# Kernel tuning notes

Measured on AMD Instinct MI355X. Metric: run time of the kernel, lower is better.

The kernel has to match this reference:

```python
import math
import jax, jax.numpy as jnp
import numpy as np

B, IMG, P, D, DEPTH, NH, HD = 8, 384, 16, 768, 12, 12, 64
NREG, NS, NF = 4, 5, 16            # registers, special tokens (1 cls + 4 reg), rope freqs
HP = IMG // P                      # 24 patches per side
NPATCH = HP * HP                   # 576
ROPE_DIM = 2 * NF                  # 32
SCALE = HD ** -0.5


def setup_inputs() -> dict:
    key = jax.random.key(0)
    ks = jax.random.split(key, 12)
    s = 0.02
    rn = lambda k, shape: (jax.random.normal(k, shape, jnp.float32) * s)
    L, DF = DEPTH, 4 * D
    inp = {
        "pixel_values": jax.random.normal(ks[0], (B, 3, IMG, IMG), jnp.float32),
        "conv_w": rn(ks[1], (D, 3, P, P)),
        "conv_b": jnp.zeros((D,), jnp.float32),
        "cls_token": rn(ks[2], (1, 1, D)),
        "storage_tokens": rn(ks[3], (1, NREG, D)),
        "periods": jnp.exp(jnp.linspace(0.0, math.log(100.0), NF)).astype(jnp.float32),
        "ln1_s": jnp.ones((L, D), jnp.float32),
        "ln1_b": jnp.zeros((L, D), jnp.float32),
        "qkv_w": rn(ks[4], (L, 3 * D, D)),
        "qkv_b": rn(ks[5], (L, 3 * D)),
        "bias_mask": jnp.zeros((L, 3 * D), jnp.float32),  # buffer init zeros -> bias nulled
        "proj_w": rn(ks[6], (L, D, D)),
        "proj_b": jnp.zeros((L, D), jnp.float32),
        "ls1": jnp.ones((L, D), jnp.float32),
        "ln2_s": jnp.ones((L, D), jnp.float32),
        "ln2_b": jnp.zeros((L, D), jnp.float32),
        "fc1_w": rn(ks[7], (L, DF, D)),
        "fc1_b": jnp.zeros((L, DF), jnp.float32),
        "fc2_w": rn(ks[8], (L, D, DF)),
        "fc2_b": jnp.zeros((L, D), jnp.float32),
        "ls2": jnp.ones((L, D), jnp.float32),
        "lnf_s": jnp.ones((D,), jnp.float32),
        "lnf_b": jnp.zeros((D,), jnp.float32),
    }
    return inp


def _ln(x, s, b):
    mu = x.mean(-1, keepdims=True)
    var = ((x - mu) ** 2).mean(-1, keepdims=True)
    return (x - mu) / jnp.sqrt(var + 1e-6) * s + b


def _rot(x, cos, sin):
    # x: [b, h, n_patch, 2*NF]; cos/sin: [n_patch, NF]; interleaved even/odd rotation
    even, odd = x[..., 0::2], x[..., 1::2]
    return jnp.stack([even * cos - odd * sin, even * sin + odd * cos], axis=-1).reshape(x.shape)


def _forward(pixel_values, conv_w, conv_b, cls_token, storage_tokens, periods,
             ln1_s, ln1_b, qkv_w, qkv_b, bias_mask, proj_w, proj_b, ls1,
             ln2_s, ln2_b, fc1_w, fc1_b, fc2_w, fc2_b, ls2, lnf_s, lnf_b):
    b = pixel_values.shape[0]
    # Patch embed: stride == kernel conv as reshape + einsum
    xp = pixel_values.reshape(b, 3, HP, P, HP, P)
    tok = jnp.einsum('bchpwq,dcpq->bhwd', xp, conv_w) + conv_b       # [b,HP,HP,D]
    tok = tok.reshape(b, NPATCH, D)
    x = jnp.concatenate([jnp.broadcast_to(cls_token, (b, 1, D)),
                         jnp.broadcast_to(storage_tokens, (b, NREG, D)), tok], axis=1)
    n = x.shape[1]

    # RoPE tables (periods buffer; freqs = 2*pi / periods)
    freqs = (2.0 * math.pi) / periods                                 # [NF]
    pos = jnp.arange(HP, dtype=jnp.float32)
    gy, gx = jnp.meshgrid(pos, pos, indexing='ij')
    ax = gx.reshape(-1, 1) * freqs                                    # [NPATCH, NF]
    ay = gy.reshape(-1, 1) * freqs
    cos_x, sin_x = jnp.cos(ax), jnp.sin(ax)
    cos_y, sin_y = jnp.cos(ay), jnp.sin(ay)

    def blk(h, p):
        (l1s, l1b, qw, qb, bm, pw, pb, g1, l2s, l2b, f1w, f1b, f2w, f2b, g2) = p
        h1 = _ln(h, l1s, l1b)
        qkv = h1 @ qw.T + qb * bm                                     # bias nulled by mask
        qkv = qkv.reshape(b, n, 3, NH, HD).transpose(2, 0, 3, 1, 4)   # [3,b,NH,n,HD]
        q, k, v = qkv[0], qkv[1], qkv[2]
        # rotary on patch tokens; rope_total == HD so the whole head is rotated
        qp, kp = q[:, :, NS:], k[:, :, NS:]
        qp = jnp.concatenate([_rot(qp[..., :ROPE_DIM], cos_x, sin_x),
                              _rot(qp[..., ROPE_DIM:], cos_y, sin_y)], axis=-1)
        kp = jnp.concatenate([_rot(kp[..., :ROPE_DIM], cos_x, sin_x),
                              _rot(kp[..., ROPE_DIM:], cos_y, sin_y)], axis=-1)
        q = jnp.concatenate([q[:, :, :NS], qp], axis=2)
        k = jnp.concatenate([k[:, :, :NS], kp], axis=2)
        attn = jax.nn.softmax(jnp.einsum('bhqd,bhkd->bhqk', q, k) * SCALE, axis=-1)
        o = jnp.einsum('bhqk,bhkd->bhqd', attn, v).transpose(0, 2, 1, 3).reshape(b, n, D)
        h = h + g1 * (o @ pw.T + pb)
        h2 = _ln(h, l2s, l2b)
        m = jax.nn.gelu(h2 @ f1w.T + f1b, approximate=False) @ f2w.T + f2b
        h = h + g2 * m
        return h, None

    params = (ln1_s, ln1_b, qkv_w, qkv_b, bias_mask, proj_w, proj_b, ls1,
              ln2_s, ln2_b, fc1_w, fc1_b, fc2_w, fc2_b, ls2)
    x, _ = jax.lax.scan(blk, x, params)
    return _ln(x, lnf_s, lnf_b)


def reference(pixel_values, conv_w, conv_b, cls_token, storage_tokens, periods,
              ln1_s, ln1_b, qkv_w, qkv_b, bias_mask, proj_w, proj_b, ls1,
              ln2_s, ln2_b, fc1_w, fc1_b, fc2_w, fc2_b, ls2, lnf_s, lnf_b):
    return _forward(pixel_values, conv_w, conv_b, cls_token, storage_tokens, periods,
                    ln1_s, ln1_b, qkv_w, qkv_b, bias_mask, proj_w, proj_b, ls1,
                    ln2_s, ln2_b, fc1_w, fc1_b, fc2_w, fc2_b, ls2, lnf_s, lnf_b)
```

## Files before the change

kernel.cpp:

```cpp
#include <hip/hip_runtime.h>
#include <math.h>

typedef unsigned short u16;
typedef __attribute__((ext_vector_type(8))) short bf8;
typedef __attribute__((ext_vector_type(4))) float f4;

#define DEV static __device__ __forceinline__

DEV u16 f2b(float f){
  unsigned u = __builtin_bit_cast(unsigned, f);
  u += 0x7fffu + ((u >> 16) & 1u);
  return (u16)(u >> 16);
}
DEV float b2f(u16 h){
  unsigned u = ((unsigned)h) << 16;
  return __builtin_bit_cast(float, u);
}

#define BATCH  8
#define NTOK   581
#define NPAD   640
#define DIM    768
#define DFF    3072
#define NHEAD  12
#define HDIM   64
#define NLAYER 12
#define MTOK   (BATCH*NTOK)
#define MPAD2  4736
#define MCONV  (BATCH*576)
#define ATTN_SCALE 0.125f
#define BHEADS (BATCH*NHEAD)
#define QSZ    ((long long)BHEADS*NPAD*HDIM)

enum { EPI_CONV=0, EPI_QKV, EPI_PROJ, EPI_GELU, EPI_FC2 };

DEV int xcdswz(int lin, int n){
  int q = n >> 3, r = n & 7;
  int x = lin & 7, o = lin >> 3;
  return (x < r ? x*(q+1) : r*(q+1) + (x - r)*q) + o;
}

template<int EPI, int BM>
__global__ __launch_bounds__(256) void gemmRS(
    const u16* __restrict__ A, int lda,
    const u16* __restrict__ B, int ldb, int K,
    const float* __restrict__ bias,
    const float* __restrict__ aux,
    float* __restrict__ Cf,
    u16* __restrict__ Cb)
{
  constexpr int MR = BM / 32;
  const int gx = gridDim.x;
  const int lin = blockIdx.y * gx + blockIdx.x;
  const int tix = xcdswz(lin, gx * gridDim.y);
  const int bm = (tix / gx) * BM, bn = (tix % gx) * 64;
  __shared__ __attribute__((aligned(16))) u16 As[2][BM][40];
  __shared__ __attribute__((aligned(16))) u16 Bs[2][64][40];
  const int tid  = threadIdx.x;
  const int lane = tid & 63, wid = tid >> 6;
  const int wr = wid >> 1, wc = wid & 1;
  const int srow = tid >> 2, scol = (tid & 3) * 8;
  const u16* gA0 = A + (long long)(bm + srow) * lda + scol;
  const u16* gA1 = A + (long long)(bm + 64 + srow) * lda + scol;
  const u16* gB  = B + (long long)(bn + srow) * ldb + scol;
  const int frow = lane & 15, quad = lane >> 4, fk = quad * 8;

  f4 acc[MR][2] = {};
  const int T = K >> 5;

  auto compute = [&](int buf){
    bf8 af[MR], bf[2];
    #pragma unroll
    for (int m = 0; m < MR; ++m)
      af[m] = *(const bf8*)&As[buf][wr*(BM/2) + m*16 + frow][fk];
    #pragma unroll
    for (int n = 0; n < 2; ++n)
      bf[n] = *(const bf8*)&Bs[buf][wc*32 + n*16 + frow][fk];
    #pragma unroll
    for (int m = 0; m < MR; ++m)
    #pragma unroll
    for (int n = 0; n < 2; ++n)
      acc[m][n] = __builtin_amdgcn_mfma_f32_16x16x32_bf16(af[m], bf[n], acc[m][n], 0, 0, 0);
  };

  bf8 xA0, xA1, xB, yA0, yA1, yB;
  xA0 = *(const bf8*)gA0;        if constexpr (BM == 128) xA1 = *(const bf8*)gA1;
  xB  = *(const bf8*)gB;
  yA0 = *(const bf8*)(gA0 + 32); if constexpr (BM == 128) yA1 = *(const bf8*)(gA1 + 32);
  yB  = *(const bf8*)(gB + 32);
  *(bf8*)&As[0][srow][scol] = xA0;
  if constexpr (BM == 128) *(bf8*)&As[0][64 + srow][scol] = xA1;
  *(bf8*)&Bs[0][srow][scol] = xB;
  __syncthreads();

  for (int t = 0; t < T; t += 2){
    if (t + 2 < T){
      xA0 = *(const bf8*)(gA0 + (t+2)*32);
      if constexpr (BM == 128) xA1 = *(const bf8*)(gA1 + (t+2)*32);
      xB  = *(const bf8*)(gB  + (t+2)*32);
    }
    *(bf8*)&As[1][srow][scol] = yA0;
    if constexpr (BM == 128) *(bf8*)&As[1][64 + srow][scol] = yA1;
    *(bf8*)&Bs[1][srow][scol] = yB;
    compute(0);
    __syncthreads();
    if (t + 3 < T){
      yA0 = *(const bf8*)(gA0 + (t+3)*32);
      if constexpr (BM == 128) yA1 = *(const bf8*)(gA1 + (t+3)*32);
      yB  = *(const bf8*)(gB  + (t+3)*32);
    }
    if (t + 2 < T){
      *(bf8*)&As[0][srow][scol] = xA0;
      if constexpr (BM == 128) *(bf8*)&As[0][64 + srow][scol] = xA1;
      *(bf8*)&Bs[0][srow][scol] = xB;
    }
    compute(1);
    __syncthreads();
  }

  #pragma unroll
  for (int mi = 0; mi < MR; ++mi)
  #pragma unroll
  for (int ni = 0; ni < 2; ++ni){
    f4 v = acc[mi][ni];
    int col = bn + wc*32 + ni*16 + frow;
    int r0  = bm + wr*(BM/2) + mi*16 + quad*4;
    #pragma unroll
    for (int j = 0; j < 4; ++j){
      int m = r0 + j;
      float val = v[j];
      if constexpr (EPI == EPI_CONV){
        int b = m / 576, p = m % 576;
        Cf[((long long)b*NTOK + 5 + p)*DIM + col] = val + bias[col];
      } else if constexpr (EPI == EPI_QKV){
        if (m < MTOK){
          int b = m / NTOK, t = m % NTOK;
          int which = col / DIM, rem = col % DIM;
          int h = rem / HDIM, hd = rem % HDIM;
          float x = val + bias[col];
          long long bh = (long long)(b*NHEAD + h);
          if (which == 0) x *= ATTN_SCALE;
          if (which == 2)
            Cb[2*QSZ + (bh*HDIM + hd)*NPAD + t] = f2b(x);
          else
            Cb[(long long)which*QSZ + (bh*NPAD + t)*HDIM + hd] = f2b(x);
        }
      } else if constexpr (EPI == EPI_PROJ || EPI == EPI_FC2){
        if (m < MTOK)
          Cf[(long long)m*DIM + col] += aux[col] * (val + bias[col]);
      } else if constexpr (EPI == EPI_GELU){
        float x = val + bias[col];
        float g = 0.5f * x * (1.0f + erff(x * 0.70710678118f));
        Cb[(long long)m*DFF + col] = f2b(g);
      }
    }
  }
}

__global__ __launch_bounds__(256) void flash_k(
    const u16* __restrict__ Q, const u16* __restrict__ K,
    const u16* __restrict__ VT, u16* __restrict__ obuf)
{
  const int qb = blockIdx.x, bh = blockIdx.y;
  const int b = bh / NHEAD, h = bh % NHEAD;
  const int tid = threadIdx.x, lane = tid & 63, w = tid >> 6;
  const int frow = lane & 15, quad = lane >> 4;
  __shared__ u16 P[4][16][80];
  const u16* Qb = Q  + (long long)bh * NPAD * HDIM;
  const u16* Kb = K  + (long long)bh * NPAD * HDIM;
  const u16* Vb = VT + (long long)bh * HDIM * NPAD;
  const bf8 qa0 = *(const bf8*)&Qb[(qb*64 + w*16 + frow)*HDIM + quad*8];
  const bf8 qa1 = *(const bf8*)&Qb[(qb*64 + w*16 + frow)*HDIM + 32 + quad*8];
  f4 o[4] = {};
  float m[4], l[4];
  #pragma unroll
  for (int j = 0; j < 4; ++j){ m[j] = -1e30f; l[j] = 0.0f; }

  for (int kt = 0; kt < NPAD/64; ++kt){
    f4 s[4];
    #pragma unroll
    for (int n = 0; n < 4; ++n){
      const u16* kr = &Kb[(kt*64 + n*16 + frow)*HDIM + quad*8];
      bf8 kb0 = *(const bf8*)kr;
      bf8 kb1 = *(const bf8*)(kr + 32);
      f4 z = {};
      z    = __builtin_amdgcn_mfma_f32_16x16x32_bf16(qa0, kb0, z, 0, 0, 0);
      s[n] = __builtin_amdgcn_mfma_f32_16x16x32_bf16(qa1, kb1, z, 0, 0, 0);
    }
    if (kt == NPAD/64 - 1){
      #pragma unroll
      for (int n = 0; n < 4; ++n){
        int kcol = kt*64 + n*16 + frow;
        if (kcol >= NTOK){ s[n][0] = s[n][1] = s[n][2] = s[n][3] = -1e30f; }
      }
    }
    float sc[4];
    #pragma unroll
    for (int j = 0; j < 4; ++j){
      float v = fmaxf(fmaxf(s[0][j], s[1][j]), fmaxf(s[2][j], s[3][j]));
      v = fmaxf(v, __shfl_xor(v, 1));  v = fmaxf(v, __shfl_xor(v, 2));
      v = fmaxf(v, __shfl_xor(v, 4));  v = fmaxf(v, __shfl_xor(v, 8));
      float mn = fmaxf(m[j], v);
      sc[j] = __expf(m[j] - mn);
      m[j] = mn;
    }
    float ts[4] = {0.f, 0.f, 0.f, 0.f};
    #pragma unroll
    for (int n = 0; n < 4; ++n){
      #pragma unroll
      for (int j = 0; j < 4; ++j){
        float p = __expf(s[n][j] - m[j]);
        ts[j] += p;
        P[w][quad*4 + j][n*16 + frow] = f2b(p);
      }
    }
    #pragma unroll
    for (int j = 0; j < 4; ++j){
      float v = ts[j];
      v += __shfl_xor(v, 1); v += __shfl_xor(v, 2);
      v += __shfl_xor(v, 4); v += __shfl_xor(v, 8);
      l[j] = l[j]*sc[j] + v;
    }
    #pragma unroll
    for (int n = 0; n < 4; ++n)
    #pragma unroll
    for (int j = 0; j < 4; ++j) o[n][j] *= sc[j];
    bf8 pa0 = *(const bf8*)&P[w][frow][quad*8];
    bf8 pa1 = *(const bf8*)&P[w][frow][quad*8 + 32];
    #pragma unroll
    for (int n = 0; n < 4; ++n){
      const u16* vr = &Vb[(n*16 + frow)*NPAD + kt*64 + quad*8];
      bf8 vb0 = *(const bf8*)vr;
      bf8 vb1 = *(const bf8*)(vr + 32);
      o[n] = __builtin_amdgcn_mfma_f32_16x16x32_bf16(pa0, vb0, o[n], 0, 0, 0);
      o[n] = __builtin_amdgcn_mfma_f32_16x16x32_bf16(pa1, vb1, o[n], 0, 0, 0);
    }
  }
  #pragma unroll
  for (int j = 0; j < 4; ++j){
    int t = qb*64 + w*16 + quad*4 + j;
    if (t < NTOK){
      float inv = 1.0f / l[j];
      #pragma unroll
      for (int n = 0; n < 4; ++n)
        obuf[((long long)b*NTOK + t)*DIM + h*HDIM + n*16 + frow] = f2b(o[n][j] * inv);
    }
  }
}

template<int F32OUT>
__global__ __launch_bounds__(256) void ln_k(const float* __restrict__ x,
    const float* __restrict__ s, const float* __restrict__ b,
    u16* __restrict__ ob, float* __restrict__ of)
{
  const long long row = blockIdx.x;
  const float* xr = x + row * DIM;
  const int t = threadIdx.x;
  float v0 = xr[t], v1 = xr[t + 256], v2 = xr[t + 512];
  float sum = v0 + v1 + v2;
  #pragma unroll
  for (int o = 32; o; o >>= 1) sum += __shfl_down(sum, o);
  __shared__ float r1[4], r2[4];
  const int lane = t & 63, w = t >> 6;
  if (lane == 0) r1[w] = sum;
  __syncthreads();
  float mu = (r1[0] + r1[1] + r1[2] + r1[3]) * (1.0f / DIM);
  float d0 = v0 - mu, d1 = v1 - mu, d2 = v2 - mu;
  float vs = d0*d0 + d1*d1 + d2*d2;
  #pragma unroll
  for (int o = 32; o; o >>= 1) vs += __shfl_down(vs, o);
  if (lane == 0) r2[w] = vs;
  __syncthreads();
  float inv = 1.0f / sqrtf((r2[0] + r2[1] + r2[2] + r2[3]) * (1.0f / DIM) + 1e-6f);
  if constexpr (F32OUT){
    float* orow = of + row * DIM;
    orow[t]       = d0 * inv * s[t]       + b[t];
    orow[t + 256] = d1 * inv * s[t + 256] + b[t + 256];
    orow[t + 512] = d2 * inv * s[t + 512] + b[t + 512];
  } else {
    u16* orow = ob + row * DIM;
    orow[t]       = f2b(d0 * inv * s[t]       + b[t]);
    orow[t + 256] = f2b(d1 * inv * s[t + 256] + b[t + 256]);
    orow[t + 512] = f2b(d2 * inv * s[t + 512] + b[t + 512]);
  }
}

__global__ void ropetab_k(const float* __restrict__ periods, float* __restrict__ tab)
{
  int idx = blockIdx.x * blockDim.x + threadIdx.x;
  if (idx >= 24 * 16) return;
  int c = idx >> 4, f = idx & 15;
  float fr = 6.283185307179586f / periods[f];
  float a = (float)c * fr;
  tab[idx]       = cosf(a);
  tab[384 + idx] = sinf(a);
}

__global__ __launch_bounds__(256) void rope_k(u16* __restrict__ Q, u16* __restrict__ K,
                                              const float* __restrict__ tab)
{
  int idx = blockIdx.x * blockDim.x + threadIdx.x;
  if (idx >= BHEADS * 576 * 32) return;
  int f  = idx & 31;
  int p  = (idx >> 5) % 576;
  int bh = idx / (576 * 32);
  int px = p % 24, py = p / 24;
  float c, s; int d0;
  if (f < 16){ c = tab[px*16 + f];        s = tab[384 + px*16 + f];        d0 = 2*f; }
  else       { int ff = f - 16;
               c = tab[py*16 + ff];       s = tab[384 + py*16 + ff];       d0 = 32 + 2*ff; }
  long long off = (((long long)bh) * NPAD + 5 + p) * HDIM + d0;
  float qe = b2f(Q[off]), qo = b2f(Q[off + 1]);
  Q[off]     = f2b(qe * c - qo * s);
  Q[off + 1] = f2b(qe * s + qo * c);
  float ke = b2f(K[off]), ko = b2f(K[off + 1]);
  K[off]     = f2b(ke * c - ko * s);
  K[off + 1] = f2b(ke * s + ko * c);
}

__global__ void initx_k(float* __restrict__ x, const float* __restrict__ cls,
                        const float* __restrict__ stor)
{
  int idx = blockIdx.x * blockDim.x + threadIdx.x;
  if (idx >= BATCH * 5 * DIM) return;
  int d = idx % DIM; int t = (idx / DIM) % 5; int b = idx / (5 * DIM);
  x[((long long)b * NTOK + t) * DIM + d] = (t == 0) ? cls[d] : stor[(t - 1) * DIM + d];
}

__global__ void patch_k(const float* __restrict__ px, u16* __restrict__ Ap)
{
  int idx = blockIdx.x * blockDim.x + threadIdx.x;
  if (idx >= MCONV * DIM) return;
  int k = idx % DIM, m = idx / DIM;
  int b = m / 576, r = m % 576, hp = r / 24, wp = r % 24;
  int c = k / 256, rem = k % 256, p = rem / 16, q = rem % 16;
  float v = px[((((long long)b * 3 + c) * 384) + hp * 16 + p) * 384 + wp * 16 + q];
  Ap[idx] = f2b(v);
}

__global__ void cvt_k(const float* __restrict__ src, u16* __restrict__ dst, long long n)
{
  long long i = (long long)blockIdx.x * blockDim.x + threadIdx.x;
  long long stride = (long long)gridDim.x * blockDim.x;
  for (; i < n; i += stride) dst[i] = f2b(src[i]);
}

__global__ void biaseff_k(const float* __restrict__ qb, const float* __restrict__ bm,
                          float* __restrict__ out, int n)
{
  int i = blockIdx.x * blockDim.x + threadIdx.x;
  if (i < n) out[i] = qb[i] * bm[i];
}

extern "C" void kernel_launch(void* const* d_in, const int* in_sizes, int n_in,
                              void* d_out, int out_size, void* d_ws, size_t ws_size,
                              hipStream_t stream)
{
  const float* pixel   = (const float*)d_in[0];
  const float* conv_w  = (const float*)d_in[1];
  const float* conv_b  = (const float*)d_in[2];
  const float* cls     = (const float*)d_in[3];
  const float* stor    = (const float*)d_in[4];
  const float* periods = (const float*)d_in[5];
  const float* ln1s    = (const float*)d_in[6];
  const float* ln1b    = (const float*)d_in[7];
  const float* qkvw    = (const float*)d_in[8];
  const float* qkvb    = (const float*)d_in[9];
  const float* bmask   = (const float*)d_in[10];
  const float* projw   = (const float*)d_in[11];
  const float* projb   = (const float*)d_in[12];
  const float* ls1     = (const float*)d_in[13];
  const float* ln2s    = (const float*)d_in[14];
  const float* ln2b    = (const float*)d_in[15];
  const float* fc1w    = (const float*)d_in[16];
  const float* fc1b    = (const float*)d_in[17];
  const float* fc2w    = (const float*)d_in[18];
  const float* fc2b    = (const float*)d_in[19];
  const float* ls2     = (const float*)d_in[20];
  const float* lnfs    = (const float*)d_in[21];
  const float* lnfb    = (const float*)d_in[22];

  char* wsp = (char*)d_ws;
  auto alloc = [&](long long bytes) -> char* {
    char* p = wsp; wsp += (bytes + 255) & ~255LL; return p;
  };
  u16*   wqkv  = (u16*)  alloc((long long)NLAYER*2304*768*2);
  u16*   wproj = (u16*)  alloc((long long)NLAYER*768*768*2);
  u16*   wfc1  = (u16*)  alloc((long long)NLAYER*3072*768*2);
  u16*   wfc2  = (u16*)  alloc((long long)NLAYER*768*3072*2);
  u16*   wconv = (u16*)  alloc((long long)768*768*2);
  float* beff  = (float*)alloc((long long)NLAYER*2304*4);
  float* x     = (float*)alloc((long long)MPAD2*DIM*4);
  u16*   h     = (u16*)  alloc((long long)MPAD2*DIM*2);
  u16*   obuf  = (u16*)  alloc((long long)MPAD2*DIM*2);
  u16*   mlp   = (u16*)  alloc((long long)MPAD2*DFF*2);
  u16*   Ap    = (u16*)  alloc((long long)MCONV*DIM*2);
  u16*   Q     = (u16*)  alloc(QSZ*2*3);
  u16*   Kb    = Q + QSZ;
  u16*   VT    = Q + 2*QSZ;
  float* tab   = (float*)alloc((long long)2*24*16*4);
  if ((size_t)(wsp - (char*)d_ws) > ws_size) return;

  auto cvt = [&](const float* src, u16* dst, long long n){
    long long nb = (n + 255) / 256; if (nb > 4096) nb = 4096;
    cvt_k<<<(int)nb, 256, 0, stream>>>(src, dst, n);
  };
  cvt(qkvw,  wqkv,  (long long)NLAYER*2304*768);
  cvt(projw, wproj, (long long)NLAYER*768*768);
  cvt(fc1w,  wfc1,  (long long)NLAYER*3072*768);
  cvt(fc2w,  wfc2,  (long long)NLAYER*768*3072);
  cvt(conv_w, wconv, (long long)768*768);
  biaseff_k<<<(NLAYER*2304 + 255)/256, 256, 0, stream>>>(qkvb, bmask, beff, NLAYER*2304);
  ropetab_k<<<2, 256, 0, stream>>>(periods, tab);
  hipMemsetAsync(Q, 0, (size_t)QSZ*2*3, stream);

  patch_k<<<(MCONV*DIM + 255)/256, 256, 0, stream>>>(pixel, Ap);
  initx_k<<<(BATCH*5*DIM + 255)/256, 256, 0, stream>>>(x, cls, stor);
  gemmRS<EPI_CONV,64><<<dim3(DIM/64, MCONV/64), 256, 0, stream>>>(
      Ap, DIM, wconv, DIM, DIM, conv_b, nullptr, x, nullptr);

  for (int l = 0; l < NLAYER; ++l){
    ln_k<0><<<MTOK, 256, 0, stream>>>(x, ln1s + l*DIM, ln1b + l*DIM, h, nullptr);
    gemmRS<EPI_QKV,128><<<dim3(2304/64, MPAD2/128), 256, 0, stream>>>(
        h, DIM, wqkv + (long long)l*2304*768, DIM, DIM,
        beff + l*2304, nullptr, nullptr, Q);
    rope_k<<<(BHEADS*576*32 + 255)/256, 256, 0, stream>>>(Q, Kb, tab);
    flash_k<<<dim3(NPAD/64, BHEADS), 256, 0, stream>>>(Q, Kb, VT, obuf);
    gemmRS<EPI_PROJ,64><<<dim3(DIM/64, MPAD2/64), 256, 0, stream>>>(
        obuf, DIM, wproj + (long long)l*768*768, DIM, DIM,
        projb + l*DIM, ls1 + l*DIM, x, nullptr);
    ln_k<0><<<MTOK, 256, 0, stream>>>(x, ln2s + l*DIM, ln2b + l*DIM, h, nullptr);
    gemmRS<EPI_GELU,128><<<dim3(DFF/64, MPAD2/128), 256, 0, stream>>>(
        h, DIM, wfc1 + (long long)l*3072*768, DIM, DIM,
        fc1b + l*DFF, nullptr, nullptr, mlp);
    gemmRS<EPI_FC2,64><<<dim3(DIM/64, MPAD2/64), 256, 0, stream>>>(
        mlp, DFF, wfc2 + (long long)l*768*3072, DFF, DFF,
        fc2b + l*DIM, ls2 + l*DIM, x, nullptr);
  }
  ln_k<1><<<MTOK, 256, 0, stream>>>(x, lnfs, lnfb, nullptr, (float*)d_out);
}
```

Measured before the change: 3.574 ms.

## Prefetch K/V tiles in registers and remap flash blocks for XCD locality

The flash attention kernel now loads the next K tile into registers while the current tile's scores are computed. It also issues the V loads at the start of each iteration so they overlap with the softmax. The grid is flattened to one dimension and decoded so that all query blocks of a given batch-head land on the same XCD, which should improve L2 reuse of K/V on MI355X. The cost is higher register pressure, which may reduce occupancy.

```diff
diff --git a/kernel.cpp b/kernel.cpp
--- a/kernel.cpp
+++ b/kernel.cpp
@@ -161,7 +161,10 @@
     const u16* __restrict__ Q, const u16* __restrict__ K,
     const u16* __restrict__ VT, u16* __restrict__ obuf)
 {
-  const int qb = blockIdx.x, bh = blockIdx.y;
+  const int lid = blockIdx.x;
+  const int xcd = lid & 7, slot = lid >> 3;
+  const int bh = xcd * 12 + slot / 10;
+  const int qb = slot % 10;
   const int b = bh / NHEAD, h = bh % NHEAD;
   const int tid = threadIdx.x, lane = tid & 63, w = tid >> 6;
   const int frow = lane & 15, quad = lane >> 4;
@@ -176,16 +179,36 @@
   #pragma unroll
   for (int j = 0; j < 4; ++j){ m[j] = -1e30f; l[j] = 0.0f; }
 
+  bf8 kb0[4], kb1[4];
+  #pragma unroll
+  for (int n = 0; n < 4; ++n){
+    const u16* kr = &Kb[(n*16 + frow)*HDIM + quad*8];
+    kb0[n] = *(const bf8*)kr;
+    kb1[n] = *(const bf8*)(kr + 32);
+  }
+
   for (int kt = 0; kt < NPAD/64; ++kt){
+    bf8 vb0[4], vb1[4];
+    #pragma unroll
+    for (int n = 0; n < 4; ++n){
+      const u16* vr = &Vb[(n*16 + frow)*NPAD + kt*64 + quad*8];
+      vb0[n] = *(const bf8*)vr;
+      vb1[n] = *(const bf8*)(vr + 32);
+    }
     f4 s[4];
     #pragma unroll
     for (int n = 0; n < 4; ++n){
-      const u16* kr = &Kb[(kt*64 + n*16 + frow)*HDIM + quad*8];
-      bf8 kb0 = *(const bf8*)kr;
-      bf8 kb1 = *(const bf8*)(kr + 32);
       f4 z = {};
-      z    = __builtin_amdgcn_mfma_f32_16x16x32_bf16(qa0, kb0, z, 0, 0, 0);
-      s[n] = __builtin_amdgcn_mfma_f32_16x16x32_bf16(qa1, kb1, z, 0, 0, 0);
+      z    = __builtin_amdgcn_mfma_f32_16x16x32_bf16(qa0, kb0[n], z, 0, 0, 0);
+      s[n] = __builtin_amdgcn_mfma_f32_16x16x32_bf16(qa1, kb1[n], z, 0, 0, 0);
+    }
+    if (kt + 1 < NPAD/64){
+      #pragma unroll
+      for (int n = 0; n < 4; ++n){
+        const u16* kr = &Kb[((kt+1)*64 + n*16 + frow)*HDIM + quad*8];
+        kb0[n] = *(const bf8*)kr;
+        kb1[n] = *(const bf8*)(kr + 32);
+      }
     }
     if (kt == NPAD/64 - 1){
       #pragma unroll
@@ -229,11 +252,8 @@
     bf8 pa1 = *(const bf8*)&P[w][frow][quad*8 + 32];
     #pragma unroll
     for (int n = 0; n < 4; ++n){
-      const u16* vr = &Vb[(n*16 + frow)*NPAD + kt*64 + quad*8];
-      bf8 vb0 = *(const bf8*)vr;
-      bf8 vb1 = *(const bf8*)(vr + 32);
-      o[n] = __builtin_amdgcn_mfma_f32_16x16x32_bf16(pa0, vb0, o[n], 0, 0, 0);
-      o[n] = __builtin_amdgcn_mfma_f32_16x16x32_bf16(pa1, vb1, o[n], 0, 0, 0);
+      o[n] = __builtin_amdgcn_mfma_f32_16x16x32_bf16(pa0, vb0[n], o[n], 0, 0, 0);
+      o[n] = __builtin_amdgcn_mfma_f32_16x16x32_bf16(pa1, vb1[n], o[n], 0, 0, 0);
     }
   }
   #pragma unroll
@@ -425,7 +445,7 @@
         h, DIM, wqkv + (long long)l*2304*768, DIM, DIM,
         beff + l*2304, nullptr, nullptr, Q);
     rope_k<<<(BHEADS*576*32 + 255)/256, 256, 0, stream>>>(Q, Kb, tab);
-    flash_k<<<dim3(NPAD/64, BHEADS), 256, 0, stream>>>(Q, Kb, VT, obuf);
+    flash_k<<<dim3(BHEADS*10), 256, 0, stream>>>(Q, Kb, VT, obuf);
     gemmRS<EPI_PROJ,64><<<dim3(DIM/64, MPAD2/64), 256, 0, stream>>>(
         obuf, DIM, wproj + (long long)l*768*768, DIM, DIM,
         projb + l*DIM, ls1 + l*DIM, x, nullptr);
```

Result: no change. 3.528 ms (-1.3%).
